# Kernel optimization log

Hardware: AMD Instinct MI355X
Metric: run time of the kernel (lower is better)

The kernel has to match this reference:

```python
import jax, jax.numpy as jnp
import numpy as np

B, L, D = 8, 4096, 128
TEMPERATURE = 1.0


def setup_inputs() -> dict:
    key = jax.random.key(0)
    kx, kw, kb = jax.random.split(key, 3)
    x = jax.random.normal(kx, (B, L, D), dtype=jnp.float32)
    # nn.Linear(dim, dim): weight [D, D], bias [D]
    bound = 1.0 / np.sqrt(D)
    W = jax.random.uniform(kw, (D, D), minval=-bound, maxval=bound, dtype=jnp.float32)
    b = jax.random.uniform(kb, (D,), minval=-bound, maxval=bound, dtype=jnp.float32)
    return {"x": x, "W": W, "b": b}


def reference(x, W, b):
    # projected = proj(x): torch Linear is x @ W.T + b
    projected = jnp.einsum("bld,ed->ble", x, W) + b            # [B, L, D]

    # adaptive_avg_pool1d over sequence length L -> L//2 (L even => pair means)
    Bq, Lx, Dx = x.shape
    q = x.reshape(Bq, Lx // 2, 2, Dx).mean(axis=2)             # [B, L/2, D]
    q = jnp.einsum("bld,ed->ble", q, W) + b                    # [B, L/2, D]

    # pairwise squared euclidean distance via ||q||^2 + ||k||^2 - 2 q.k (GEMM form)
    q_sq = jnp.sum(q * q, axis=-1, keepdims=True)              # [B, L/2, 1]
    k_sq = jnp.sum(projected * projected, axis=-1)[:, None, :] # [B, 1, L]
    qk = jnp.einsum("bqd,bkd->bqk", q, projected)              # [B, L/2, L]
    power = jnp.maximum(q_sq + k_sq - 2.0 * qk, 0.0)
    distances = jnp.sqrt(power)
    similarities = jnp.exp(-distances * TEMPERATURE)           # [B, L/2, L]

    k = jnp.einsum("bqk,bkd->bqd", similarities, projected)    # [B, L/2, D]
    v = k
    return (q, k, v)
```

## Files before the change

### kernel.cpp

```cpp
#include <hip/hip_runtime.h>
#include <hip/hip_bf16.h>
#include <stdint.h>

#define NB 8
#define LL 4096
#define LQ 2048
#define DD 128

typedef __attribute__((ext_vector_type(8))) short short8;
typedef __attribute__((ext_vector_type(4))) short short4v;
typedef __attribute__((ext_vector_type(4))) float f4;
typedef __attribute__((ext_vector_type(2))) unsigned int u2;

typedef const __attribute__((address_space(1))) unsigned int guint_t;
typedef __attribute__((address_space(3))) unsigned int luint_t;

__device__ __forceinline__ short8 pack8(const float* v) {
    __hip_bfloat16 h[8];
    #pragma unroll
    for (int j = 0; j < 8; ++j) h[j] = __float2bfloat16(v[j]);
    return *(short8*)h;
}

__global__ __launch_bounds__(256) void projA_kernel(
    const float* __restrict__ x, const float* __restrict__ W,
    const float* __restrict__ bias,
    __hip_bfloat16* __restrict__ proj_sw, __hip_bfloat16* __restrict__ projT,
    __hip_bfloat16* __restrict__ qb, float* __restrict__ qf,
    float* __restrict__ psq, float* __restrict__ qsq)
{
    __shared__ __hip_bfloat16 Wlds[128 * 128];
    __shared__ __hip_bfloat16 Tt[4][128 * 16];

    const int tid = threadIdx.x;
    const int lane = tid & 63, w = tid >> 6;
    const int lr = lane & 15, lh = lane >> 4;

    #pragma unroll
    for (int k = 0; k < 16; ++k) {
        const int f = k * 1024 + tid * 4;
        const int e = f >> 7, col = f & 127;
        f4 v = *(const f4*)&W[f];
        __hip_bfloat16 h[4];
        #pragma unroll
        for (int j = 0; j < 4; ++j) h[j] = __float2bfloat16(v[j]);
        const int byte = e * 256 + (((col * 2)) ^ ((e & 7) << 4));
        *(u2*)((char*)Wlds + byte) = *(u2*)h;
    }
    float bv[8];
    #pragma unroll
    for (int nt = 0; nt < 8; ++nt) bv[nt] = bias[nt * 16 + lr];
    __syncthreads();

    const int tile = blockIdx.x;
    const int row0 = tile * 64 + w * 16;
    const bool qmode = tile >= (NB * LL / 64);

    short8 a[4];
    if (!qmode) {
        const float* src = x + (size_t)(row0 + lr) * DD;
        #pragma unroll
        for (int ks = 0; ks < 4; ++ks) {
            float t[8];
            *(f4*)&t[0] = *(const f4*)&src[ks * 32 + lh * 8];
            *(f4*)&t[4] = *(const f4*)&src[ks * 32 + lh * 8 + 4];
            a[ks] = pack8(t);
        }
    } else {
        const int gq = row0 - NB * LL + lr;
        const int b = gq >> 11, l = gq & 2047;
        const float* s0 = x + ((size_t)b * LL + 2 * l) * DD;
        #pragma unroll
        for (int ks = 0; ks < 4; ++ks) {
            float t[8];
            f4 u0 = *(const f4*)&s0[ks * 32 + lh * 8];
            f4 u1 = *(const f4*)&s0[ks * 32 + lh * 8 + 4];
            f4 v0 = *(const f4*)&s0[DD + ks * 32 + lh * 8];
            f4 v1 = *(const f4*)&s0[DD + ks * 32 + lh * 8 + 4];
            *(f4*)&t[0] = (u0 + v0) * 0.5f;
            *(f4*)&t[4] = (u1 + v1) * 0.5f;
            a[ks] = pack8(t);
        }
    }

    f4 acc[8] = {};
    #pragma unroll
    for (int nt = 0; nt < 8; ++nt) {
        const int e = nt * 16 + lr;
        #pragma unroll
        for (int ks = 0; ks < 4; ++ks) {
            const int byte = e * 256 + ((ks * 64 + lh * 16) ^ ((lr & 7) << 4));
            short8 bk = *(const short8*)((char*)Wlds + byte);
            acc[nt] = __builtin_amdgcn_mfma_f32_16x16x32_bf16(a[ks], bk, acc[nt], 0, 0, 0);
        }
    }

    __hip_bfloat16 h[8][4];
    f4 rn = {0.f, 0.f, 0.f, 0.f};
    #pragma unroll
    for (int nt = 0; nt < 8; ++nt)
        #pragma unroll
        for (int r = 0; r < 4; ++r) {
            float v = acc[nt][r] + bv[nt];
            acc[nt][r] = v;
            h[nt][r] = __float2bfloat16(v);
            float vb = __bfloat162float(h[nt][r]);
            rn[r] += vb * vb;
        }
    #pragma unroll
    for (int m = 1; m < 16; m <<= 1) {
        #pragma unroll
        for (int r = 0; r < 4; ++r) rn[r] += __shfl_xor(rn[r], m);
    }

    if (!qmode) {
        const int gr = row0;
        #pragma unroll
        for (int nt = 0; nt < 8; ++nt)
            #pragma unroll
            for (int r = 0; r < 4; ++r) {
                const int row = gr + lh * 4 + r;
                const int byte = (nt * 32 + lr * 2) ^ (((lh * 4 + r) & 7) << 4);
                *(__hip_bfloat16*)((char*)proj_sw + (size_t)row * 256 + byte) = h[nt][r];
            }
        if (lr == 0) *(f4*)&psq[gr + lh * 4] = rn;
        #pragma unroll
        for (int nt = 0; nt < 8; ++nt) {
            __hip_bfloat16 p[4] = {h[nt][0], h[nt][1], h[nt][2], h[nt][3]};
            *(u2*)((char*)&Tt[w][0] + (nt * 16 + lr) * 32 + lh * 8) = *(u2*)p;
        }
        const int b = gr >> 12, l0 = gr & 4095;
        #pragma unroll
        for (int i = 0; i < 2; ++i) {
            const int e = lane + i * 64;
            short8 t0 = *(const short8*)&Tt[w][e * 16];
            short8 t1 = *(const short8*)&Tt[w][e * 16 + 8];
            __hip_bfloat16* dst = projT + ((size_t)(b * DD + e)) * LL + l0;
            *(short8*)dst = t0;
            *(short8*)(dst + 8) = t1;
        }
    } else {
        const int gq = row0 - NB * LL;
        #pragma unroll
        for (int nt = 0; nt < 8; ++nt)
            #pragma unroll
            for (int r = 0; r < 4; ++r) {
                const size_t idx = (size_t)(gq + lh * 4 + r) * DD + nt * 16 + lr;
                qb[idx] = h[nt][r];
                qf[idx] = acc[nt][r];
            }
        if (lr == 0) *(f4*)&qsq[gq + lh * 4] = rn;
    }
}

__global__ __launch_bounds__(512, 2) void fused_kernel(
    const __hip_bfloat16* __restrict__ proj_sw, const __hip_bfloat16* __restrict__ projT,
    const __hip_bfloat16* __restrict__ qb, const float* __restrict__ psq,
    const float* __restrict__ qsq,
    float* __restrict__ pp0, float* __restrict__ pp1,
    float* __restrict__ pp2, float* __restrict__ pp3, int keys_per)
{
    __shared__ __hip_bfloat16 pbuf[2][4096];
    __shared__ __hip_bfloat16 tbuf[2][128 * 40];
    __shared__ float psbuf[2048];

    const int bid = blockIdx.x;
    const int b = bid & 7;
    const int qt8 = (bid >> 3) & 7;
    const int ks = bid >> 6;
    const int tid = threadIdx.x;
    const int w = tid >> 6, lane = tid & 63;
    const int lr = lane & 15, lh = lane >> 4;

    const int qrow0 = qt8 * 256 + w * 32;
    const int key0 = ks * keys_per;
    const int ntiles = keys_per / 32;

    const char* psw = (const char*)proj_sw + (size_t)b * LL * 256;
    const __hip_bfloat16* ptb = projT + (size_t)b * DD * LL;
    const float* psb = psq + b * LL;

    for (int i = tid; i < keys_per; i += 512) psbuf[i] = psb[key0 + i];

    short8 aq[2][4];
    const __hip_bfloat16* qbase = qb + ((size_t)b * LQ + qrow0) * DD;
    #pragma unroll
    for (int qt = 0; qt < 2; ++qt)
        #pragma unroll
        for (int kss = 0; kss < 4; ++kss)
            aq[qt][kss] = *(const short8*)&qbase[(size_t)(qt * 16 + lr) * DD + kss * 32 + lh * 8];
    float qn[2] = { qsq[b * LQ + qrow0 + lr], qsq[b * LQ + qrow0 + 16 + lr] };

    const int sd = tid >> 2, ss = tid & 3;

    __builtin_amdgcn_global_load_lds(
        (guint_t*)(psw + (size_t)key0 * 256 + w * 1024 + lane * 16),
        (luint_t*)&pbuf[0][w * 512], 16, 0, 0);
    {
        short8 t0 = *(const short8*)(ptb + (size_t)sd * LL + key0 + ss * 8);
        *(short8*)((char*)tbuf[0] + sd * 80 + ss * 16) = t0;
    }
    __syncthreads();

    f4 oc[2][8] = {};
    int p = 0;

    for (int t = 0; t < ntiles; ++t) {
        short8 tnext;
        if (t + 1 < ntiles) {
            __builtin_amdgcn_global_load_lds(
                (guint_t*)(psw + (size_t)(key0 + (t + 1) * 32) * 256 + w * 1024 + lane * 16),
                (luint_t*)&pbuf[p ^ 1][w * 512], 16, 0, 0);
            tnext = *(const short8*)(ptb + (size_t)sd * LL + key0 + (t + 1) * 32 + ss * 8);
        }

        f4 s[2][2] = {};
        #pragma unroll
        for (int kss = 0; kss < 4; ++kss) {
            const int off = kss * 64 + lh * 16;
            short8 ak0 = *(const short8*)((char*)pbuf[p] + lr * 256 + (off ^ ((lr & 7) << 4)));
            short8 ak1 = *(const short8*)((char*)pbuf[p] + (16 + lr) * 256 + (off ^ ((lr & 7) << 4)));
            s[0][0] = __builtin_amdgcn_mfma_f32_16x16x32_bf16(ak0, aq[0][kss], s[0][0], 0, 0, 0);
            s[0][1] = __builtin_amdgcn_mfma_f32_16x16x32_bf16(ak0, aq[1][kss], s[0][1], 0, 0, 0);
            s[1][0] = __builtin_amdgcn_mfma_f32_16x16x32_bf16(ak1, aq[0][kss], s[1][0], 0, 0, 0);
            s[1][1] = __builtin_amdgcn_mfma_f32_16x16x32_bf16(ak1, aq[1][kss], s[1][1], 0, 0, 0);
        }

        f4 pn0 = *(const f4*)&psbuf[t * 32 + lh * 4];
        f4 pn1 = *(const f4*)&psbuf[t * 32 + 16 + lh * 4];
        short8 pa[2];
        #pragma unroll
        for (int qt = 0; qt < 2; ++qt) {
            __hip_bfloat16 hh[8];
            #pragma unroll
            for (int r = 0; r < 4; ++r) {
                float p0 = fmaxf(qn[qt] + pn0[r] - 2.0f * s[0][qt][r], 1e-20f);
                float p1 = fmaxf(qn[qt] + pn1[r] - 2.0f * s[1][qt][r], 1e-20f);
                float d0 = p0 * __frsqrt_rn(p0);
                float d1 = p1 * __frsqrt_rn(p1);
                hh[r]     = __float2bfloat16(__expf(-d0));
                hh[4 + r] = __float2bfloat16(__expf(-d1));
            }
            pa[qt] = *(short8*)hh;
        }

        #pragma unroll
        for (int dt = 0; dt < 8; ++dt) {
            const char* rowp = (const char*)tbuf[p] + (dt * 16 + lr) * 80;
            union { short8 v; short4v h[2]; } u;
            u.h[0] = *(const short4v*)(rowp + lh * 8);
            u.h[1] = *(const short4v*)(rowp + 32 + lh * 8);
            oc[0][dt] = __builtin_amdgcn_mfma_f32_16x16x32_bf16(pa[0], u.v, oc[0][dt], 0, 0, 0);
            oc[1][dt] = __builtin_amdgcn_mfma_f32_16x16x32_bf16(pa[1], u.v, oc[1][dt], 0, 0, 0);
        }

        if (t + 1 < ntiles)
            *(short8*)((char*)tbuf[p ^ 1] + sd * 80 + ss * 16) = tnext;
        __syncthreads();
        p ^= 1;
    }

    float* pb = (ks == 0) ? pp0 : (ks == 1) ? pp1 : (ks == 2) ? pp2 : pp3;
    #pragma unroll
    for (int qt = 0; qt < 2; ++qt)
        #pragma unroll
        for (int dt = 0; dt < 8; ++dt)
            #pragma unroll
            for (int r = 0; r < 4; ++r)
                pb[((size_t)b * LQ + qrow0 + qt * 16 + lh * 4 + r) * DD + dt * 16 + lr] = oc[qt][dt][r];
}

__global__ __launch_bounds__(256) void reduce_kernel(
    const float* __restrict__ p0, const float* __restrict__ p1,
    const float* __restrict__ p2, const float* __restrict__ p3,
    float* __restrict__ outk, float* __restrict__ outv, int nsplit)
{
    const int b = blockIdx.x & 7;
    const size_t j = (size_t)b * (LQ * DD) + ((size_t)(blockIdx.x >> 3) * 256 + threadIdx.x) * 4;
    f4 v = *(const f4*)&p0[j] + *(const f4*)&p1[j];
    if (nsplit == 4) v += *(const f4*)&p2[j] + *(const f4*)&p3[j];
    *(f4*)&outk[j] = v;
    *(f4*)&outv[j] = v;
}

extern "C" void kernel_launch(void* const* d_in, const int* in_sizes, int n_in,
                              void* d_out, int out_size, void* d_ws, size_t ws_size,
                              hipStream_t stream) {
    const float* x = (const float*)d_in[0];
    const float* W = (const float*)d_in[1];
    const float* bias = (const float*)d_in[2];

    float* out = (float*)d_out;
    const size_t NQ = (size_t)NB * LQ * DD;
    float* qf = out;
    float* outk = out + NQ;
    float* outv = out + 2 * NQ;

    char* ws = (char*)d_ws;
    __hip_bfloat16* proj  = (__hip_bfloat16*)ws;
    __hip_bfloat16* projT = (__hip_bfloat16*)(ws + 8u * 1024 * 1024);
    __hip_bfloat16* qb    = (__hip_bfloat16*)(ws + 16u * 1024 * 1024);
    float* psq            = (float*)(ws + 20u * 1024 * 1024);
    float* qsq            = (float*)(ws + 20u * 1024 * 1024 + 256u * 1024);
    float* pw2            = (float*)(ws + 24u * 1024 * 1024);
    float* pw3            = (float*)(ws + 32u * 1024 * 1024);

    const int nsplit = (ws_size >= (40ull << 20)) ? 4 : 2;
    const int keys_per = LL / nsplit;

    hipLaunchKernelGGL(projA_kernel, dim3((NB * LL + NB * LQ) / 64), dim3(256), 0, stream,
                       x, W, bias, proj, projT, qb, qf, psq, qsq);
    hipLaunchKernelGGL(fused_kernel, dim3(64 * nsplit), dim3(512), 0, stream,
                       proj, projT, qb, psq, qsq, outk, outv, pw2, pw3, keys_per);
    hipLaunchKernelGGL(reduce_kernel, dim3(2048), dim3(256), 0, stream,
                       outk, outv, pw2, pw3, outk, outv, nsplit);
}
```

Baseline: 87.31 us.

## Halve per-wave query rows in fused kernel to double grid and occupancy

```diff
diff --git a/kernel.cpp b/kernel.cpp
--- a/kernel.cpp
+++ b/kernel.cpp
@@ -153,7 +153,7 @@
     }
 }
 
-__global__ __launch_bounds__(512, 2) void fused_kernel(
+__global__ __launch_bounds__(512, 4) void fused_kernel(
     const __hip_bfloat16* __restrict__ proj_sw, const __hip_bfloat16* __restrict__ projT,
     const __hip_bfloat16* __restrict__ qb, const float* __restrict__ psq,
     const float* __restrict__ qsq,
@@ -161,18 +161,18 @@
     float* __restrict__ pp2, float* __restrict__ pp3, int keys_per)
 {
     __shared__ __hip_bfloat16 pbuf[2][4096];
-    __shared__ __hip_bfloat16 tbuf[2][128 * 40];
+    __shared__ __hip_bfloat16 tbuf[2][128 * 36];
     __shared__ float psbuf[2048];
 
     const int bid = blockIdx.x;
     const int b = bid & 7;
-    const int qt8 = (bid >> 3) & 7;
-    const int ks = bid >> 6;
+    const int qt16 = (bid >> 3) & 15;
+    const int ks = bid >> 7;
     const int tid = threadIdx.x;
     const int w = tid >> 6, lane = tid & 63;
     const int lr = lane & 15, lh = lane >> 4;
 
-    const int qrow0 = qt8 * 256 + w * 32;
+    const int qrow0 = qt16 * 128 + w * 16;
     const int key0 = ks * keys_per;
     const int ntiles = keys_per / 32;
 
@@ -182,14 +182,12 @@
 
     for (int i = tid; i < keys_per; i += 512) psbuf[i] = psb[key0 + i];
 
-    short8 aq[2][4];
+    short8 aq[4];
     const __hip_bfloat16* qbase = qb + ((size_t)b * LQ + qrow0) * DD;
     #pragma unroll
-    for (int qt = 0; qt < 2; ++qt)
-        #pragma unroll
-        for (int kss = 0; kss < 4; ++kss)
-            aq[qt][kss] = *(const short8*)&qbase[(size_t)(qt * 16 + lr) * DD + kss * 32 + lh * 8];
-    float qn[2] = { qsq[b * LQ + qrow0 + lr], qsq[b * LQ + qrow0 + 16 + lr] };
+    for (int kss = 0; kss < 4; ++kss)
+        aq[kss] = *(const short8*)&qbase[(size_t)lr * DD + kss * 32 + lh * 8];
+    const float qn = qsq[b * LQ + qrow0 + lr];
 
     const int sd = tid >> 2, ss = tid & 3;
 
@@ -198,11 +196,11 @@
         (luint_t*)&pbuf[0][w * 512], 16, 0, 0);
     {
         short8 t0 = *(const short8*)(ptb + (size_t)sd * LL + key0 + ss * 8);
-        *(short8*)((char*)tbuf[0] + sd * 80 + ss * 16) = t0;
+        *(short8*)((char*)tbuf[0] + sd * 72 + ss * 16) = t0;
     }
     __syncthreads();
 
-    f4 oc[2][8] = {};
+    f4 oc[8] = {};
     int p = 0;
 
     for (int t = 0; t < ntiles; ++t) {
@@ -214,60 +212,54 @@
             tnext = *(const short8*)(ptb + (size_t)sd * LL + key0 + (t + 1) * 32 + ss * 8);
         }
 
-        f4 s[2][2] = {};
+        f4 s[2] = {};
         #pragma unroll
         for (int kss = 0; kss < 4; ++kss) {
             const int off = kss * 64 + lh * 16;
             short8 ak0 = *(const short8*)((char*)pbuf[p] + lr * 256 + (off ^ ((lr & 7) << 4)));
             short8 ak1 = *(const short8*)((char*)pbuf[p] + (16 + lr) * 256 + (off ^ ((lr & 7) << 4)));
-            s[0][0] = __builtin_amdgcn_mfma_f32_16x16x32_bf16(ak0, aq[0][kss], s[0][0], 0, 0, 0);
-            s[0][1] = __builtin_amdgcn_mfma_f32_16x16x32_bf16(ak0, aq[1][kss], s[0][1], 0, 0, 0);
-            s[1][0] = __builtin_amdgcn_mfma_f32_16x16x32_bf16(ak1, aq[0][kss], s[1][0], 0, 0, 0);
-            s[1][1] = __builtin_amdgcn_mfma_f32_16x16x32_bf16(ak1, aq[1][kss], s[1][1], 0, 0, 0);
+            s[0] = __builtin_amdgcn_mfma_f32_16x16x32_bf16(ak0, aq[kss], s[0], 0, 0, 0);
+            s[1] = __builtin_amdgcn_mfma_f32_16x16x32_bf16(ak1, aq[kss], s[1], 0, 0, 0);
         }
 
         f4 pn0 = *(const f4*)&psbuf[t * 32 + lh * 4];
         f4 pn1 = *(const f4*)&psbuf[t * 32 + 16 + lh * 4];
-        short8 pa[2];
-        #pragma unroll
-        for (int qt = 0; qt < 2; ++qt) {
+        short8 pa;
+        {
             __hip_bfloat16 hh[8];
             #pragma unroll
             for (int r = 0; r < 4; ++r) {
-                float p0 = fmaxf(qn[qt] + pn0[r] - 2.0f * s[0][qt][r], 1e-20f);
-                float p1 = fmaxf(qn[qt] + pn1[r] - 2.0f * s[1][qt][r], 1e-20f);
+                float p0 = fmaxf(qn + pn0[r] - 2.0f * s[0][r], 1e-20f);
+                float p1 = fmaxf(qn + pn1[r] - 2.0f * s[1][r], 1e-20f);
                 float d0 = p0 * __frsqrt_rn(p0);
                 float d1 = p1 * __frsqrt_rn(p1);
                 hh[r]     = __float2bfloat16(__expf(-d0));
                 hh[4 + r] = __float2bfloat16(__expf(-d1));
             }
-            pa[qt] = *(short8*)hh;
+            pa = *(short8*)hh;
         }
 
         #pragma unroll
         for (int dt = 0; dt < 8; ++dt) {
-            const char* rowp = (const char*)tbuf[p] + (dt * 16 + lr) * 80;
+            const char* rowp = (const char*)tbuf[p] + (dt * 16 + lr) * 72;
             union { short8 v; short4v h[2]; } u;
             u.h[0] = *(const short4v*)(rowp + lh * 8);
             u.h[1] = *(const short4v*)(rowp + 32 + lh * 8);
-            oc[0][dt] = __builtin_amdgcn_mfma_f32_16x16x32_bf16(pa[0], u.v, oc[0][dt], 0, 0, 0);
-            oc[1][dt] = __builtin_amdgcn_mfma_f32_16x16x32_bf16(pa[1], u.v, oc[1][dt], 0, 0, 0);
+            oc[dt] = __builtin_amdgcn_mfma_f32_16x16x32_bf16(pa, u.v, oc[dt], 0, 0, 0);
         }
 
         if (t + 1 < ntiles)
-            *(short8*)((char*)tbuf[p ^ 1] + sd * 80 + ss * 16) = tnext;
+            *(short8*)((char*)tbuf[p ^ 1] + sd * 72 + ss * 16) = tnext;
         __syncthreads();
         p ^= 1;
     }
 
     float* pb = (ks == 0) ? pp0 : (ks == 1) ? pp1 : (ks == 2) ? pp2 : pp3;
     #pragma unroll
-    for (int qt = 0; qt < 2; ++qt)
-        #pragma unroll
-        for (int dt = 0; dt < 8; ++dt)
-            #pragma unroll
-            for (int r = 0; r < 4; ++r)
-                pb[((size_t)b * LQ + qrow0 + qt * 16 + lh * 4 + r) * DD + dt * 16 + lr] = oc[qt][dt][r];
+    for (int dt = 0; dt < 8; ++dt)
+        #pragma unroll
+        for (int r = 0; r < 4; ++r)
+            pb[((size_t)b * LQ + qrow0 + lh * 4 + r) * DD + dt * 16 + lr] = oc[dt][r];
 }
 
 __global__ __launch_bounds__(256) void reduce_kernel(
@@ -310,7 +302,7 @@
 
     hipLaunchKernelGGL(projA_kernel, dim3((NB * LL + NB * LQ) / 64), dim3(256), 0, stream,
                        x, W, bias, proj, projT, qb, qf, psq, qsq);
-    hipLaunchKernelGGL(fused_kernel, dim3(64 * nsplit), dim3(512), 0, stream,
+    hipLaunchKernelGGL(fused_kernel, dim3(128 * nsplit), dim3(512), 0, stream,
                        proj, projT, qb, psq, qsq, outk, outv, pw2, pw3, keys_per);
     hipLaunchKernelGGL(reduce_kernel, dim3(2048), dim3(256), 0, stream,
                        outk, outv, pw2, pw3, outk, outv, nsplit);
```

Result: faster. 79.89 us (-8.5%).
